# Performance work log

Hardware: AMD Instinct MI355X
Metric: run time of the kernel (lower is better)

The kernel has to match this reference:

```python
import jax, jax.numpy as jnp
import numpy as np

NUM_INPUTS = 376
NUM_ACTIONS = 17
L1, L2 = 256, 128
BHID = 128
NE = 2
B = 65536


def setup_inputs() -> dict:
    key = jax.random.key(0)
    ks = jax.random.split(key, 16)
    s = lambda k, shape: jax.random.normal(k, shape, dtype=jnp.float32) * 0.05
    return {
        "states": jax.random.normal(ks[0], (B, NUM_INPUTS), dtype=jnp.float32),
        # blending module params
        "bw1": s(ks[1], (BHID, NUM_INPUTS)), "bb1": s(ks[2], (BHID,)),
        "bw2": s(ks[3], (BHID, BHID)),       "bb2": s(ks[4], (BHID,)),
        "bwo": s(ks[5], (NE, BHID)),         "bbo": s(ks[6], (NE,)),
        # stacked expert (p1, p2) policy params, leading axis = expert
        "ew1": s(ks[7], (NE, L1, NUM_INPUTS)), "eb1": s(ks[8], (NE, L1)),
        "ew2": s(ks[9], (NE, L2, L1)),         "eb2": s(ks[10], (NE, L2)),
        "ewm": s(ks[11], (NE, NUM_ACTIONS, L2)), "ebm": s(ks[12], (NE, NUM_ACTIONS)),
    }


def _blended_linear(h, coeffs, W, b):
    # Linear with per-sample blended weights: (sum_e c_e W_e) h + sum_e c_e b_e
    # == sum_e c_e (W_e h + b_e), so compute both expert outputs and blend.
    y = jnp.einsum('bi,eoi->beo', h, W) + b[None]  # [B, E, O]
    return jnp.einsum('be,beo->bo', coeffs, y)


def reference(states, bw1, bb1, bw2, bb2, bwo, bbo, ew1, eb1, ew2, eb2, ewm, ebm):
    # BlendingModule: 2-layer relu MLP -> softmax over experts
    g = jax.nn.relu(states @ bw1.T + bb1)
    g = jax.nn.relu(g @ bw2.T + bb2)
    coeffs = jax.nn.softmax(g @ bwo.T + bbo, axis=-1)  # [B, 2]
    # Per-sample blended PolicyModule (256 -> 128 -> actions, tanh head)
    h = jax.nn.relu(_blended_linear(states, coeffs, ew1, eb1))
    h = jax.nn.relu(_blended_linear(h, coeffs, ew2, eb2))
    mu = jnp.tanh(_blended_linear(h, coeffs, ewm, ebm))
    return mu
```

## Files before the change

kernel.cpp:

```cpp
#include <hip/hip_runtime.h>
#include <math.h>


typedef __attribute__((ext_vector_type(8))) _Float16 half8;
typedef __attribute__((ext_vector_type(4))) _Float16 half4;
typedef __attribute__((ext_vector_type(4))) float    f32x4;

#define MFMA16(a, b, c) __builtin_amdgcn_mfma_f32_16x16x32_f16((a), (b), (c), 0, 0, 0)
#define SWZ(row) (((row) & 7) << 4)

#define MT 32
#define T  512

#define S_B      0
#define G1_B     24576
#define G2_B     32768
#define H1_B     24576
#define H2_B     24576
#define LDS_BYTES 40960

#define WS_W1 0
#define WS_W2 49152
#define WS_E1 65536
#define WS_E2 262144
#define WS_EM 327680
#define WS_HALFS 335872
#define WS_BYTES 671744

__device__ __forceinline__ half8 cvt8(const float* __restrict__ p) {
    const float4 a = *reinterpret_cast<const float4*>(p);
    const float4 b = *reinterpret_cast<const float4*>(p + 4);
    half8 r;
    r[0] = (_Float16)a.x; r[1] = (_Float16)a.y; r[2] = (_Float16)a.z; r[3] = (_Float16)a.w;
    r[4] = (_Float16)b.x; r[5] = (_Float16)b.y; r[6] = (_Float16)b.z; r[7] = (_Float16)b.w;
    return r;
}

__global__ __launch_bounds__(256)
void prep_weights(const float* __restrict__ bw1, const float* __restrict__ bw2,
                  const float* __restrict__ ew1, const float* __restrict__ ew2,
                  const float* __restrict__ ewm, _Float16* __restrict__ wsw)
{
    const int i = blockIdx.x * 256 + threadIdx.x;
    if (i >= WS_HALFS) return;
    const float* W; int N, K, KC, j0;
    if      (i < 49152)  { W = bw1; N = 128; K = 376; KC = 12; j0 = i - WS_W1; }
    else if (i < 65536)  { W = bw2; N = 128; K = 128; KC = 4;  j0 = i - WS_W2; }
    else if (i < 262144) { W = ew1; N = 512; K = 376; KC = 12; j0 = i - WS_E1; }
    else if (i < 327680) { W = ew2; N = 256; K = 256; KC = 8;  j0 = i - WS_E2; }
    else                 { W = ewm; N = 34;  K = 128; KC = 4;  j0 = i - WS_EM; }
    const int tile = j0 >> 9;
    const int rem  = j0 & 511;
    const int l    = rem >> 3;
    const int jj   = rem & 7;
    const int n0   = tile / KC, kc = tile - n0 * KC;
    int n = n0 * 16 + (l & 15);
    const int k = kc * 32 + (l >> 4) * 8 + jj;
    float v = 0.f;
    if (W == ewm) {
        const int e = n >> 5, a = n & 31;
        if (a < 17 && k < K) v = ewm[(e * 17 + a) * K + k];
    } else {
        if (n < N && k < K) v = W[n * K + k];
    }
    wsw[i] = (_Float16)v;
}

template <bool USE_WS>
__global__ __launch_bounds__(512)
__attribute__((amdgpu_waves_per_eu(4)))
void actor_kernel(const float* __restrict__ states,
                  const float* __restrict__ bw1, const float* __restrict__ bb1,
                  const float* __restrict__ bw2, const float* __restrict__ bb2,
                  const float* __restrict__ bwo, const float* __restrict__ bbo,
                  const float* __restrict__ ew1, const float* __restrict__ eb1,
                  const float* __restrict__ ew2, const float* __restrict__ eb2,
                  const float* __restrict__ ewm, const float* __restrict__ ebm,
                  const _Float16* __restrict__ wsw,
                  float* __restrict__ out)
{
    extern __shared__ char smc[];
    const int t    = threadIdx.x;
    const int l    = t & 63;
    const int l15  = l & 15;
    const int kgrp = l >> 4;
    const int kg16 = kgrp * 16;
    const int wv   = __builtin_amdgcn_readfirstlane(t >> 6);
    const int base = blockIdx.x * MT;
    const int lB   = l * 8;

    const half8 zf = {0,0,0,0,0,0,0,0};

    {
        const float4* src = reinterpret_cast<const float4*>(states + (long)base * 376);
        for (int q = t; q < MT * 94; q += T) {
            const int r  = q / 94;
            const int c4 = q - r * 94;
            const float4 v = src[q];
            half4 h;
            h[0] = (_Float16)v.x; h[1] = (_Float16)v.y;
            h[2] = (_Float16)v.z; h[3] = (_Float16)v.w;
            *(half4*)(smc + S_B + ((r * 768 + c4 * 8) ^ SWZ(r))) = h;
        }
        if (t < MT) {
            *(float4*)(smc + S_B + ((t * 768 + 752) ^ SWZ(t))) = make_float4(0.f, 0.f, 0.f, 0.f);
        }
    }
    __syncthreads();

    {
        f32x4 acc[2] = {{0,0,0,0},{0,0,0,0}};
        const int col = wv * 16 + l15;
        for (int kc = 0; kc < 12; ++kc) {
            half8 bf;
            if constexpr (USE_WS) bf = *(const half8*)(wsw + WS_W1 + (wv * 12 + kc) * 512 + lB);
            else {
                const int g = kc * 4 + kgrp;
                bf = (g < 47) ? cvt8(bw1 + col * 376 + g * 8) : zf;
            }
            const int koff = kc * 64 + kg16;
            #pragma unroll
            for (int mt = 0; mt < 2; ++mt) {
                const int row = mt * 16 + l15;
                const half8 af = *(const half8*)(smc + S_B + ((row * 768 + koff) ^ SWZ(row)));
                acc[mt] = MFMA16(af, bf, acc[mt]);
            }
        }
        const float bias = bb1[col];
        #pragma unroll
        for (int mt = 0; mt < 2; ++mt) {
            #pragma unroll
            for (int j = 0; j < 4; ++j) {
                const int row = mt * 16 + kgrp * 4 + j;
                const float v = fmaxf(acc[mt][j] + bias, 0.f);
                *(_Float16*)(smc + G1_B + ((row * 256 + col * 2) ^ SWZ(row))) = (_Float16)v;
            }
        }
    }
    __syncthreads();

    {
        f32x4 acc[2] = {{0,0,0,0},{0,0,0,0}};
        const int col = wv * 16 + l15;
        for (int kc = 0; kc < 4; ++kc) {
            half8 bf;
            if constexpr (USE_WS) bf = *(const half8*)(wsw + WS_W2 + (wv * 4 + kc) * 512 + lB);
            else                  bf = cvt8(bw2 + col * 128 + (kc * 4 + kgrp) * 8);
            const int koff = kc * 64 + kg16;
            #pragma unroll
            for (int mt = 0; mt < 2; ++mt) {
                const int row = mt * 16 + l15;
                const half8 af = *(const half8*)(smc + G1_B + ((row * 256 + koff) ^ SWZ(row)));
                acc[mt] = MFMA16(af, bf, acc[mt]);
            }
        }
        const float bias = bb2[col];
        #pragma unroll
        for (int mt = 0; mt < 2; ++mt) {
            #pragma unroll
            for (int j = 0; j < 4; ++j) {
                const int row = mt * 16 + kgrp * 4 + j;
                const float v = fmaxf(acc[mt][j] + bias, 0.f);
                *(_Float16*)(smc + G2_B + ((row * 256 + col * 2) ^ SWZ(row))) = (_Float16)v;
            }
        }
    }
    __syncthreads();

    if (t < MT) {
        float z0 = bbo[0], z1 = bbo[1];
        for (int k8 = 0; k8 < 16; ++k8) {
            const half8 hv = *(const half8*)(smc + G2_B + ((t * 256 + k8 * 16) ^ SWZ(t)));
            #pragma unroll
            for (int j = 0; j < 8; ++j) {
                const float g = (float)hv[j];
                z0 = fmaf(g, bwo[k8 * 8 + j], z0);
                z1 = fmaf(g, bwo[128 + k8 * 8 + j], z1);
            }
        }
        const float m  = fmaxf(z0, z1);
        const float e0 = __expf(z0 - m), e1 = __expf(z1 - m);
        const float inv = 1.f / (e0 + e1);
        const float c0 = e0 * inv, c1 = e1 * inv;
        half4 cc;
        cc[0] = (_Float16)c0; cc[1] = (_Float16)(c0 - (float)cc[0]);
        cc[2] = (_Float16)c1; cc[3] = (_Float16)(c1 - (float)cc[2]);
        *(half4*)(smc + S_B + ((t * 768 + 752) ^ SWZ(t))) = cc;
    }
    __syncthreads();

    {
        f32x4 aA[2][2], aB[2][2];
        #pragma unroll
        for (int nt = 0; nt < 2; ++nt)
            #pragma unroll
            for (int mt = 0; mt < 2; ++mt) { aA[nt][mt] = {0,0,0,0}; aB[nt][mt] = {0,0,0,0}; }

        for (int kc = 0; kc < 12; ++kc) {
            const int koff = kc * 64 + kg16;
            half8 af[2];
            #pragma unroll
            for (int mt = 0; mt < 2; ++mt) {
                const int row = mt * 16 + l15;
                af[mt] = *(const half8*)(smc + S_B + ((row * 768 + koff) ^ SWZ(row)));
            }
            #pragma unroll
            for (int nt = 0; nt < 2; ++nt) {
                half8 b0, b1;
                if constexpr (USE_WS) {
                    const int n0 = wv * 2 + nt;
                    b0 = *(const half8*)(wsw + WS_E1 + (n0 * 12 + kc) * 512 + lB);
                    b1 = *(const half8*)(wsw + WS_E1 + ((16 + n0) * 12 + kc) * 512 + lB);
                } else {
                    const int g = kc * 4 + kgrp;
                    const int wr = wv * 32 + nt * 16 + l15;
                    b0 = (g < 47) ? cvt8(ew1 + wr * 376 + g * 8)         : zf;
                    b1 = (g < 47) ? cvt8(ew1 + (wr + 256) * 376 + g * 8) : zf;
                }
                #pragma unroll
                for (int mt = 0; mt < 2; ++mt) {
                    aA[nt][mt] = MFMA16(af[mt], b0, aA[nt][mt]);
                    aB[nt][mt] = MFMA16(af[mt], b1, aB[nt][mt]);
                }
            }
        }
        #pragma unroll
        for (int nt = 0; nt < 2; ++nt) {
            const int col = wv * 32 + nt * 16 + l15;
            const float b0 = eb1[col], b1 = eb1[256 + col];
            #pragma unroll
            for (int mt = 0; mt < 2; ++mt) {
                #pragma unroll
                for (int j = 0; j < 4; ++j) {
                    const int row = mt * 16 + kgrp * 4 + j;
                    const half4 cc = *(const half4*)(smc + S_B + ((row * 768 + 752) ^ SWZ(row)));
                    const float c0 = (float)cc[0] + (float)cc[1];
                    const float c1 = (float)cc[2] + (float)cc[3];
                    float v = c0 * (aA[nt][mt][j] + b0) + c1 * (aB[nt][mt][j] + b1);
                    v = fmaxf(v, 0.f);
                    *(_Float16*)(smc + H1_B + ((row * 512 + col * 2) ^ SWZ(row))) = (_Float16)v;
                }
            }
        }
    }
    __syncthreads();

    {
        f32x4 cA[2], cB[2];
        #pragma unroll
        for (int mt = 0; mt < 2; ++mt) { cA[mt] = {0,0,0,0}; cB[mt] = {0,0,0,0}; }
        const int col = wv * 16 + l15;
        for (int kc = 0; kc < 8; ++kc) {
            half8 b0, b1;
            if constexpr (USE_WS) {
                b0 = *(const half8*)(wsw + WS_E2 + (wv * 8 + kc) * 512 + lB);
                b1 = *(const half8*)(wsw + WS_E2 + ((8 + wv) * 8 + kc) * 512 + lB);
            } else {
                const int g = kc * 4 + kgrp;
                b0 = cvt8(ew2 + col * 256 + g * 8);
                b1 = cvt8(ew2 + (col + 128) * 256 + g * 8);
            }
            const int koff = kc * 64 + kg16;
            #pragma unroll
            for (int mt = 0; mt < 2; ++mt) {
                const int row = mt * 16 + l15;
                const half8 af = *(const half8*)(smc + H1_B + ((row * 512 + koff) ^ SWZ(row)));
                cA[mt] = MFMA16(af, b0, cA[mt]);
                cB[mt] = MFMA16(af, b1, cB[mt]);
            }
        }
        __syncthreads();
        const float b0 = eb2[col], b1 = eb2[128 + col];
        #pragma unroll
        for (int mt = 0; mt < 2; ++mt) {
            #pragma unroll
            for (int j = 0; j < 4; ++j) {
                const int row = mt * 16 + kgrp * 4 + j;
                const half4 cc = *(const half4*)(smc + S_B + ((row * 768 + 752) ^ SWZ(row)));
                const float c0 = (float)cc[0] + (float)cc[1];
                const float c1 = (float)cc[2] + (float)cc[3];
                float v = c0 * (cA[mt][j] + b0) + c1 * (cB[mt][j] + b1);
                v = fmaxf(v, 0.f);
                *(_Float16*)(smc + H2_B + ((row * 256 + col * 2) ^ SWZ(row))) = (_Float16)v;
            }
        }
    }
    __syncthreads();

    if (wv < 4) {
        const int colt = wv & 1;
        const int mt   = wv >> 1;
        f32x4 c0a = {0,0,0,0}, c1a = {0,0,0,0};
        const int col  = colt * 16 + l15;
        const bool vcol = (col < 17);
        const int arow = mt * 16 + l15;
        for (int kc = 0; kc < 4; ++kc) {
            const int koff = kc * 64 + kg16;
            const half8 af = *(const half8*)(smc + H2_B + ((arow * 256 + koff) ^ SWZ(arow)));
            half8 b0, b1;
            if constexpr (USE_WS) {
                b0 = *(const half8*)(wsw + WS_EM + (colt * 4 + kc) * 512 + lB);
                b1 = *(const half8*)(wsw + WS_EM + ((2 + colt) * 4 + kc) * 512 + lB);
            } else {
                const int g = kc * 4 + kgrp;
                b0 = vcol ? cvt8(ewm + col * 128 + g * 8)        : zf;
                b1 = vcol ? cvt8(ewm + (17 + col) * 128 + g * 8) : zf;
            }
            c0a = MFMA16(af, b0, c0a);
            c1a = MFMA16(af, b1, c1a);
        }
        if (vcol) {
            const float b0 = ebm[col], b1 = ebm[17 + col];
            #pragma unroll
            for (int j = 0; j < 4; ++j) {
                const int row = mt * 16 + kgrp * 4 + j;
                const half4 cc = *(const half4*)(smc + S_B + ((row * 768 + 752) ^ SWZ(row)));
                const float c0 = (float)cc[0] + (float)cc[1];
                const float c1 = (float)cc[2] + (float)cc[3];
                const float v = c0 * (c0a[j] + b0) + c1 * (c1a[j] + b1);
                out[(long)(base + row) * 17 + col] = tanhf(v);
            }
        }
    }
}

extern "C" void kernel_launch(void* const* d_in, const int* in_sizes, int n_in,
                              void* d_out, int out_size, void* d_ws, size_t ws_size,
                              hipStream_t stream) {
    (void)in_sizes; (void)n_in; (void)out_size;
    const float* states = (const float*)d_in[0];
    const float* bw1 = (const float*)d_in[1];
    const float* bb1 = (const float*)d_in[2];
    const float* bw2 = (const float*)d_in[3];
    const float* bb2 = (const float*)d_in[4];
    const float* bwo = (const float*)d_in[5];
    const float* bbo = (const float*)d_in[6];
    const float* ew1 = (const float*)d_in[7];
    const float* eb1 = (const float*)d_in[8];
    const float* ew2 = (const float*)d_in[9];
    const float* eb2 = (const float*)d_in[10];
    const float* ewm = (const float*)d_in[11];
    const float* ebm = (const float*)d_in[12];
    float* out = (float*)d_out;

    const int nblk = 65536 / MT;

    if (d_ws != nullptr && ws_size >= (size_t)WS_BYTES) {
        _Float16* wsw = (_Float16*)d_ws;
        prep_weights<<<dim3((WS_HALFS + 255) / 256), dim3(256), 0, stream>>>(
            bw1, bw2, ew1, ew2, ewm, wsw);
        actor_kernel<true><<<dim3(nblk), dim3(T), LDS_BYTES, stream>>>(
            states, bw1, bb1, bw2, bb2, bwo, bbo,
            ew1, eb1, ew2, eb2, ewm, ebm, wsw, out);
    } else {
        actor_kernel<false><<<dim3(nblk), dim3(T), LDS_BYTES, stream>>>(
            states, bw1, bb1, bw2, bb2, bwo, bbo,
            ew1, eb1, ew2, eb2, ewm, ebm, nullptr, out);
    }
}
```

Baseline: 96.08 us.

## Prefetch weight fragments one k-step ahead and parallelize blend softmax across all threads

Adds register double-buffering of the global weight fragments in each MFMA GEMM loop: the fragment for the next k-chunk is loaded while the current one feeds the MFMAs, and the loops are fully unrolled. The blending-head dot product, previously done serially by 32 threads, is now spread over all 512 threads with shuffle reductions. The occupancy hint is relaxed from 4 to 2 waves per EU, which gives the compiler more registers for the prefetched values but may reduce latency hiding across waves.

New measurement: 86.82 us. 9.6% less time.

```diff
diff --git a/kernel.cpp b/kernel.cpp
--- a/kernel.cpp
+++ b/kernel.cpp
@@ -68,7 +68,7 @@
 
 template <bool USE_WS>
 __global__ __launch_bounds__(512)
-__attribute__((amdgpu_waves_per_eu(4)))
+__attribute__((amdgpu_waves_per_eu(2)))
 void actor_kernel(const float* __restrict__ states,
                   const float* __restrict__ bw1, const float* __restrict__ bb1,
                   const float* __restrict__ bw2, const float* __restrict__ bb2,
@@ -111,19 +111,21 @@
     {
         f32x4 acc[2] = {{0,0,0,0},{0,0,0,0}};
         const int col = wv * 16 + l15;
+        auto ldW = [&](int kc) -> half8 {
+            if constexpr (USE_WS) return *(const half8*)(wsw + WS_W1 + (wv * 12 + kc) * 512 + lB);
+            else { const int g = kc * 4 + kgrp; return (g < 47) ? cvt8(bw1 + col * 376 + g * 8) : zf; }
+        };
+        half8 bf = ldW(0);
+        #pragma unroll
         for (int kc = 0; kc < 12; ++kc) {
-            half8 bf;
-            if constexpr (USE_WS) bf = *(const half8*)(wsw + WS_W1 + (wv * 12 + kc) * 512 + lB);
-            else {
-                const int g = kc * 4 + kgrp;
-                bf = (g < 47) ? cvt8(bw1 + col * 376 + g * 8) : zf;
-            }
+            const half8 cur = bf;
+            if (kc < 11) bf = ldW(kc + 1);
             const int koff = kc * 64 + kg16;
             #pragma unroll
             for (int mt = 0; mt < 2; ++mt) {
                 const int row = mt * 16 + l15;
                 const half8 af = *(const half8*)(smc + S_B + ((row * 768 + koff) ^ SWZ(row)));
-                acc[mt] = MFMA16(af, bf, acc[mt]);
+                acc[mt] = MFMA16(af, cur, acc[mt]);
             }
         }
         const float bias = bb1[col];
@@ -142,16 +144,21 @@
     {
         f32x4 acc[2] = {{0,0,0,0},{0,0,0,0}};
         const int col = wv * 16 + l15;
+        auto ldW = [&](int kc) -> half8 {
+            if constexpr (USE_WS) return *(const half8*)(wsw + WS_W2 + (wv * 4 + kc) * 512 + lB);
+            else                  return cvt8(bw2 + col * 128 + (kc * 4 + kgrp) * 8);
+        };
+        half8 bf = ldW(0);
+        #pragma unroll
         for (int kc = 0; kc < 4; ++kc) {
-            half8 bf;
-            if constexpr (USE_WS) bf = *(const half8*)(wsw + WS_W2 + (wv * 4 + kc) * 512 + lB);
-            else                  bf = cvt8(bw2 + col * 128 + (kc * 4 + kgrp) * 8);
+            const half8 cur = bf;
+            if (kc < 3) bf = ldW(kc + 1);
             const int koff = kc * 64 + kg16;
             #pragma unroll
             for (int mt = 0; mt < 2; ++mt) {
                 const int row = mt * 16 + l15;
                 const half8 af = *(const half8*)(smc + G1_B + ((row * 256 + koff) ^ SWZ(row)));
-                acc[mt] = MFMA16(af, bf, acc[mt]);
+                acc[mt] = MFMA16(af, cur, acc[mt]);
             }
         }
         const float bias = bb2[col];
@@ -167,25 +174,38 @@
     }
     __syncthreads();
 
-    if (t < MT) {
-        float z0 = bbo[0], z1 = bbo[1];
-        for (int k8 = 0; k8 < 16; ++k8) {
-            const half8 hv = *(const half8*)(smc + G2_B + ((t * 256 + k8 * 16) ^ SWZ(t)));
-            #pragma unroll
-            for (int j = 0; j < 8; ++j) {
-                const float g = (float)hv[j];
-                z0 = fmaf(g, bwo[k8 * 8 + j], z0);
-                z1 = fmaf(g, bwo[128 + k8 * 8 + j], z1);
-            }
-        }
-        const float m  = fmaxf(z0, z1);
-        const float e0 = __expf(z0 - m), e1 = __expf(z1 - m);
-        const float inv = 1.f / (e0 + e1);
-        const float c0 = e0 * inv, c1 = e1 * inv;
-        half4 cc;
-        cc[0] = (_Float16)c0; cc[1] = (_Float16)(c0 - (float)cc[0]);
-        cc[2] = (_Float16)c1; cc[3] = (_Float16)(c1 - (float)cc[2]);
-        *(half4*)(smc + S_B + ((t * 768 + 752) ^ SWZ(t))) = cc;
+    {
+        const int s     = t >> 4;
+        const int r     = t & 15;
+        const int e     = r & 1;
+        const int chunk = r >> 1;
+        float z = 0.f;
+        const float* wo = bwo + e * 128 + chunk * 16;
+        #pragma unroll
+        for (int q = 0; q < 2; ++q) {
+            const half8 hv = *(const half8*)(smc + G2_B + ((s * 256 + chunk * 32 + q * 16) ^ SWZ(s)));
+            const float4 w0 = *(const float4*)(wo + q * 8);
+            const float4 w1 = *(const float4*)(wo + q * 8 + 4);
+            z = fmaf((float)hv[0], w0.x, z); z = fmaf((float)hv[1], w0.y, z);
+            z = fmaf((float)hv[2], w0.z, z); z = fmaf((float)hv[3], w0.w, z);
+            z = fmaf((float)hv[4], w1.x, z); z = fmaf((float)hv[5], w1.y, z);
+            z = fmaf((float)hv[6], w1.z, z); z = fmaf((float)hv[7], w1.w, z);
+        }
+        z += __shfl_xor(z, 2, 64);
+        z += __shfl_xor(z, 4, 64);
+        z += __shfl_xor(z, 8, 64);
+        z += bbo[e];
+        const float zo = __shfl_xor(z, 1, 64);
+        if (r < 2) {
+            const float m = fmaxf(z, zo);
+            const float ea = __expf(z - m), eb = __expf(zo - m);
+            const float c_self = ea / (ea + eb);
+            const _Float16 ch = (_Float16)c_self;
+            const _Float16 cl = (_Float16)(c_self - (float)ch);
+            union { _Float16 h[2]; unsigned u; } pk;
+            pk.h[0] = ch; pk.h[1] = cl;
+            *(unsigned*)(smc + S_B + (((s * 768 + 752) ^ SWZ(s)) + e * 4)) = pk.u;
+        }
     }
     __syncthreads();
 
@@ -196,32 +216,34 @@
             #pragma unroll
             for (int mt = 0; mt < 2; ++mt) { aA[nt][mt] = {0,0,0,0}; aB[nt][mt] = {0,0,0,0}; }
 
+        auto ldE1 = [&](int kc, int nt, int ex) -> half8 {
+            if constexpr (USE_WS) {
+                const int n0 = wv * 2 + nt + ex * 16;
+                return *(const half8*)(wsw + WS_E1 + (n0 * 12 + kc) * 512 + lB);
+            } else {
+                const int g = kc * 4 + kgrp;
+                const int wr = wv * 32 + nt * 16 + l15 + ex * 256;
+                return (g < 47) ? cvt8(ew1 + wr * 376 + g * 8) : zf;
+            }
+        };
+        half8 b00 = ldE1(0, 0, 0), b01 = ldE1(0, 0, 1);
+        half8 b10 = ldE1(0, 1, 0), b11 = ldE1(0, 1, 1);
+        #pragma unroll
         for (int kc = 0; kc < 12; ++kc) {
-            const int koff = kc * 64 + kg16;
-            half8 af[2];
+            const half8 c00 = b00, c01 = b01, c10 = b10, c11 = b11;
+            if (kc < 11) {
+                b00 = ldE1(kc + 1, 0, 0); b01 = ldE1(kc + 1, 0, 1);
+                b10 = ldE1(kc + 1, 1, 0); b11 = ldE1(kc + 1, 1, 1);
+            }
+            const int koff = kc * 64 + kg16;
             #pragma unroll
             for (int mt = 0; mt < 2; ++mt) {
                 const int row = mt * 16 + l15;
-                af[mt] = *(const half8*)(smc + S_B + ((row * 768 + koff) ^ SWZ(row)));
-            }
-            #pragma unroll
-            for (int nt = 0; nt < 2; ++nt) {
-                half8 b0, b1;
-                if constexpr (USE_WS) {
-                    const int n0 = wv * 2 + nt;
-                    b0 = *(const half8*)(wsw + WS_E1 + (n0 * 12 + kc) * 512 + lB);
-                    b1 = *(const half8*)(wsw + WS_E1 + ((16 + n0) * 12 + kc) * 512 + lB);
-                } else {
-                    const int g = kc * 4 + kgrp;
-                    const int wr = wv * 32 + nt * 16 + l15;
-                    b0 = (g < 47) ? cvt8(ew1 + wr * 376 + g * 8)         : zf;
-                    b1 = (g < 47) ? cvt8(ew1 + (wr + 256) * 376 + g * 8) : zf;
-                }
-                #pragma unroll
-                for (int mt = 0; mt < 2; ++mt) {
-                    aA[nt][mt] = MFMA16(af[mt], b0, aA[nt][mt]);
-                    aB[nt][mt] = MFMA16(af[mt], b1, aB[nt][mt]);
-                }
+                const half8 af = *(const half8*)(smc + S_B + ((row * 768 + koff) ^ SWZ(row)));
+                aA[0][mt] = MFMA16(af, c00, aA[0][mt]);
+                aB[0][mt] = MFMA16(af, c01, aB[0][mt]);
+                aA[1][mt] = MFMA16(af, c10, aA[1][mt]);
+                aB[1][mt] = MFMA16(af, c11, aB[1][mt]);
             }
         }
         #pragma unroll
@@ -250,27 +272,30 @@
         #pragma unroll
         for (int mt = 0; mt < 2; ++mt) { cA[mt] = {0,0,0,0}; cB[mt] = {0,0,0,0}; }
         const int col = wv * 16 + l15;
-        for (int kc = 0; kc < 8; ++kc) {
-            half8 b0, b1;
+        auto ldE2 = [&](int kc, int ex) -> half8 {
             if constexpr (USE_WS) {
-                b0 = *(const half8*)(wsw + WS_E2 + (wv * 8 + kc) * 512 + lB);
-                b1 = *(const half8*)(wsw + WS_E2 + ((8 + wv) * 8 + kc) * 512 + lB);
+                return *(const half8*)(wsw + WS_E2 + ((wv + ex * 8) * 8 + kc) * 512 + lB);
             } else {
                 const int g = kc * 4 + kgrp;
-                b0 = cvt8(ew2 + col * 256 + g * 8);
-                b1 = cvt8(ew2 + (col + 128) * 256 + g * 8);
-            }
+                return cvt8(ew2 + (col + ex * 128) * 256 + g * 8);
+            }
+        };
+        half8 b0 = ldE2(0, 0), b1 = ldE2(0, 1);
+        #pragma unroll
+        for (int kc = 0; kc < 8; ++kc) {
+            const half8 c0f = b0, c1f = b1;
+            if (kc < 7) { b0 = ldE2(kc + 1, 0); b1 = ldE2(kc + 1, 1); }
             const int koff = kc * 64 + kg16;
             #pragma unroll
             for (int mt = 0; mt < 2; ++mt) {
                 const int row = mt * 16 + l15;
                 const half8 af = *(const half8*)(smc + H1_B + ((row * 512 + koff) ^ SWZ(row)));
-                cA[mt] = MFMA16(af, b0, cA[mt]);
-                cB[mt] = MFMA16(af, b1, cB[mt]);
+                cA[mt] = MFMA16(af, c0f, cA[mt]);
+                cB[mt] = MFMA16(af, c1f, cB[mt]);
             }
         }
         __syncthreads();
-        const float b0 = eb2[col], b1 = eb2[128 + col];
+        const float b0s = eb2[col], b1s = eb2[128 + col];
         #pragma unroll
         for (int mt = 0; mt < 2; ++mt) {
             #pragma unroll
@@ -279,7 +304,7 @@
                 const half4 cc = *(const half4*)(smc + S_B + ((row * 768 + 752) ^ SWZ(row)));
                 const float c0 = (float)cc[0] + (float)cc[1];
                 const float c1 = (float)cc[2] + (float)cc[3];
-                float v = c0 * (cA[mt][j] + b0) + c1 * (cB[mt][j] + b1);
+                float v = c0 * (cA[mt][j] + b0s) + c1 * (cB[mt][j] + b1s);
                 v = fmaxf(v, 0.f);
                 *(_Float16*)(smc + H2_B + ((row * 256 + col * 2) ^ SWZ(row))) = (_Float16)v;
             }
```
